# Performance work log

Hardware: AMD Instinct MI355X
Metric: run time of the kernel (lower is better)

The kernel has to match this reference:

```python
import jax, jax.numpy as jnp
import numpy as np

TEMP = 0.1
GROUPS = 16
EPS = 1e-5
COS_EPS = 1e-8


def _encoder(x, conv_w, conv_b, gn_g, gn_b):
    # Conv2d(C,C,3,pad=1) -> GroupNorm(16,C) -> ReLU -> AdaptiveAvgPool2d(1) -> Flatten
    y = jax.lax.conv_general_dilated(
        x, conv_w, window_strides=(1, 1), padding='SAME',
        dimension_numbers=('NCHW', 'OIHW', 'NCHW')) + conv_b[None, :, None, None]
    B, C, H, W = y.shape
    yg = y.reshape(B, GROUPS, C // GROUPS, H, W)
    mu = yg.mean(axis=(2, 3, 4), keepdims=True)
    var = yg.var(axis=(2, 3, 4), keepdims=True)
    yn = ((yg - mu) * jax.lax.rsqrt(var + EPS)).reshape(B, C, H, W)
    y = yn * gn_g[None, :, None, None] + gn_b[None, :, None, None]
    y = jax.nn.relu(y)
    return y.mean(axis=(2, 3))  # [B, C]


def _projector(h, w1, b1, w2, b2, ln_g, ln_b):
    h = jax.nn.relu(h @ w1 + b1)
    h = h @ w2 + b2
    mu = h.mean(axis=-1, keepdims=True)
    var = h.var(axis=-1, keepdims=True)
    return (h - mu) * jax.lax.rsqrt(var + EPS) * ln_g + ln_b


def _predictor(z, w1, b1, w2, b2):
    return jax.nn.relu(z @ w1 + b1) @ w2 + b2


def _l2norm(z):
    n = jnp.sqrt(jnp.sum(z * z, axis=1, keepdims=True))
    return z / jnp.maximum(n, COS_EPS)


def _pair_loss(zi, zj, off_idx):
    # vectorized version of the nested-loop cosine-sim + cross-entropy (label 0)
    S = (_l2norm(zi) @ _l2norm(zj).T) / TEMP  # [B, B]
    pos = jnp.diagonal(S)                     # sim(i_k, j_k)
    neg = jnp.take_along_axis(S, off_idx, axis=1)  # [B, B-1], row k = S[k, l!=k]
    logits = jnp.concatenate([pos[:, None], neg], axis=1)
    return jnp.mean(jax.nn.logsumexp(logits, axis=1) - logits[:, 0])


def setup_inputs() -> dict:
    key = jax.random.key(0)
    ks = jax.random.split(key, 32)
    B, C, H, W, P = 256, 256, 16, 16, 128
    d = {}
    d['x_t2w'] = jax.random.normal(ks[0], (B, C, H, W), jnp.float32)
    d['x_t2f'] = jax.random.normal(ks[1], (B, C, H, W), jnp.float32)
    d['x_t1n'] = jax.random.normal(ks[2], (B, C, H, W), jnp.float32)
    i = 3
    for m in ('t2w', 't2f', 't1n'):
        d[f'conv_w_{m}'] = jax.random.normal(ks[i], (C, C, 3, 3), jnp.float32) * 0.02; i += 1
        d[f'conv_b_{m}'] = jnp.zeros((C,), jnp.float32)
        d[f'gn_g_{m}'] = jnp.ones((C,), jnp.float32)
        d[f'gn_b_{m}'] = jnp.zeros((C,), jnp.float32)
    d['proj_w1'] = jax.random.normal(ks[i], (C, C), jnp.float32) * 0.02; i += 1
    d['proj_b1'] = jnp.zeros((C,), jnp.float32)
    d['proj_w2'] = jax.random.normal(ks[i], (C, P), jnp.float32) * 0.02; i += 1
    d['proj_b2'] = jnp.zeros((P,), jnp.float32)
    d['ln_g'] = jnp.ones((P,), jnp.float32)
    d['ln_b'] = jnp.zeros((P,), jnp.float32)
    d['pred_w1'] = jax.random.normal(ks[i], (P, P), jnp.float32) * 0.02; i += 1
    d['pred_b1'] = jnp.zeros((P,), jnp.float32)
    d['pred_w2'] = jax.random.normal(ks[i], (P, P), jnp.float32) * 0.02; i += 1
    d['pred_b2'] = jnp.zeros((P,), jnp.float32)
    return d


def reference(x_t2w, x_t2f, x_t1n,
              conv_w_t2w, conv_b_t2w, gn_g_t2w, gn_b_t2w,
              conv_w_t2f, conv_b_t2f, gn_g_t2f, gn_b_t2f,
              conv_w_t1n, conv_b_t1n, gn_g_t1n, gn_b_t1n,
              proj_w1, proj_b1, proj_w2, proj_b2, ln_g, ln_b,
              pred_w1, pred_b1, pred_w2, pred_b2):
    xs = [x_t2w, x_t2f, x_t1n]
    enc_params = [(conv_w_t2w, conv_b_t2w, gn_g_t2w, gn_b_t2w),
                  (conv_w_t2f, conv_b_t2f, gn_g_t2f, gn_b_t2f),
                  (conv_w_t1n, conv_b_t1n, gn_g_t1n, gn_b_t1n)]
    encoded = [_encoder(x, *p) for x, p in zip(xs, enc_params)]
    projected = [_projector(e, proj_w1, proj_b1, proj_w2, proj_b2, ln_g, ln_b) for e in encoded]
    preds = [_predictor(z, pred_w1, pred_b1, pred_w2, pred_b2) for z in projected]

    B = projected[0].shape[0]
    off_idx = jnp.asarray(np.array([[l for l in range(B) if l != k] for k in range(B)],
                                    dtype=np.int32))
    pairs = [(0, 1), (0, 2), (1, 2)]
    loss = sum(_pair_loss(projected[i], projected[j], off_idx) for i, j in pairs) / len(pairs)

    return (jnp.stack(encoded), jnp.stack(projected), jnp.stack(preds), loss)
```

## Files before the change

### kernel.cpp

```cpp
#include <hip/hip_runtime.h>
#include <hip/hip_bf16.h>

typedef float f32x4 __attribute__((ext_vector_type(4)));
typedef __bf16 bf16x8 __attribute__((ext_vector_type(8)));
typedef unsigned short u16x8 __attribute__((ext_vector_type(8)));

#define GN_EPS 1e-5f
#define LN_EPS 1e-5f
#define COS_EPS_F 1e-8f

__device__ __forceinline__ unsigned short f2bf(float f) {
  unsigned int u = __builtin_bit_cast(unsigned int, f);
  u += 0x7fffu + ((u >> 16) & 1u);
  return (unsigned short)(u >> 16);
}

__global__ void transpose_kernel(const float* __restrict__ x0,
                                 const float* __restrict__ x1,
                                 const float* __restrict__ x2,
                                 unsigned short* __restrict__ xT,
                                 unsigned int strideElems, int mBase) {
  __shared__ float lds[64][129];
  int m = mBase + (blockIdx.x >> 11);
  int bid = blockIdx.x & 2047;
  const float* x = (m == 0) ? x0 : ((m == 1) ? x1 : x2);
  unsigned short* dst = xT + (unsigned int)(m - mBase) * strideElems;

  int hwt = bid & 3, cit = (bid >> 2) & 1, b = bid >> 3;
  int hw0 = hwt * 64, ci0 = cit * 128;
  int tid = threadIdx.x;

  int hwx = tid & 63, cy0 = tid >> 6;
  const float* xb = x + (b * 256 + ci0) * 256 + hw0;
  #pragma unroll 8
  for (int p = 0; p < 32; ++p) {
    int cy = cy0 + 4 * p;
    lds[hwx][cy] = xb[cy * 256 + hwx];
  }
  __syncthreads();

  int cp = tid & 63, hy0 = tid >> 6;
  unsigned int* outp = (unsigned int*)(dst + (b * 256 + hw0) * 256 + ci0);
  #pragma unroll 4
  for (int p = 0; p < 16; ++p) {
    int hy = hy0 + 4 * p;
    float lo = lds[hy][2 * cp];
    float hi = lds[hy][2 * cp + 1];
    unsigned int w = ((unsigned int)f2bf(hi) << 16) | f2bf(lo);
    outp[hy * 128 + cp] = w;
  }
}

__global__ void pack_kernel(const float* __restrict__ w0,
                            const float* __restrict__ w1,
                            const float* __restrict__ w2,
                            unsigned short* __restrict__ wp,
                            unsigned short* __restrict__ zerobuf) {
  int m = blockIdx.y;
  const float* w = (m == 0) ? w0 : ((m == 1) ? w1 : w2);
  int idx = blockIdx.x * 256 + threadIdx.x;
  if (m == 0 && blockIdx.x == 0 && threadIdx.x < 256) zerobuf[threadIdx.x] = 0;
  int ci = idx & 255;
  int rest = idx >> 8;
  int khw = rest % 9, co = rest / 9;
  wp[m * 589824 + idx] = f2bf(w[(co * 256 + ci) * 9 + khw]);
}

__device__ __forceinline__ void gl_lds16(const unsigned short* g, unsigned short* l) {
  __builtin_amdgcn_global_load_lds(
      (const __attribute__((address_space(1))) void*)g,
      (__attribute__((address_space(3))) void*)l, 16, 0, 0);
}

__launch_bounds__(512, 2)
__global__ void conv_gn_pool(const unsigned short* __restrict__ xT,
                             unsigned int xTstride,
                             const unsigned short* __restrict__ wp,
                             const unsigned short* __restrict__ zb,
                             const float* __restrict__ cb0, const float* __restrict__ cb1,
                             const float* __restrict__ cb2,
                             const float* __restrict__ gg0, const float* __restrict__ gg1,
                             const float* __restrict__ gg2,
                             const float* __restrict__ gb0, const float* __restrict__ gb1,
                             const float* __restrict__ gb2,
                             float* __restrict__ enc, int mBase) {
  __shared__ unsigned short Ab[4][8192];
  __shared__ unsigned short Bb[4][8192];
  __shared__ float gsum[16], gsq[16], pooled[256];

  int mm = mBase + (blockIdx.x >> 8);
  int bb = blockIdx.x & 255;
  int b = (bb & 7) * 32 + (bb >> 3);
  const float* cbias = (mm == 0) ? cb0 : ((mm == 1) ? cb1 : cb2);
  const float* gng   = (mm == 0) ? gg0 : ((mm == 1) ? gg1 : gg2);
  const float* gnb   = (mm == 0) ? gb0 : ((mm == 1) ? gb1 : gb2);

  int tid = threadIdx.x;
  int wid = tid >> 6, lane = tid & 63;
  int wr = wid >> 2, wc = wid & 3;
  int l15 = lane & 15, l4 = lane >> 4;

  if (tid < 16) { gsum[tid] = 0.f; gsq[tid] = 0.f; }
  if (tid < 256) pooled[tid] = 0.f;

  int s0 = tid, s1 = 512 + tid;
  int r0 = s0 >> 2, c0 = s0 & 3;
  int r1 = s1 >> 2, c1 = s1 & 3;
  int cs0 = (c0 ^ ((r0 >> 1) & 3)) * 8;
  int cs1 = (c1 ^ ((r1 >> 1) & 3)) * 8;
  int rh0 = r0 >> 4, rw0 = r0 & 15;
  int rh1 = r1 >> 4, rw1 = r1 & 15;

  const unsigned short* xb = xT + (unsigned int)(mm - mBase) * xTstride + b * 65536;
  const unsigned short* wpm = wp + mm * 589824;
  const unsigned short* bB0 = wpm + r0 * 2304 + cs0;
  const unsigned short* bB1 = wpm + r1 * 2304 + cs1;

  int kch = (l4 ^ ((l15 >> 1) & 3)) * 8;
  int base_af = (wr * 128 + l15) * 32 + kch;
  int base_bf = (wc * 64 + l15) * 32 + kch;

  f32x4 acc[8][4];
  #pragma unroll
  for (int i = 0; i < 8; ++i)
    #pragma unroll
    for (int j = 0; j < 4; ++j) acc[i][j] = (f32x4)(0.0f);

  #define STAGE_A(T2)                                                          \
    {                                                                          \
      int khw_ = (T2) >> 3, kc_ = (T2) & 7;                                    \
      int kh_ = khw_ / 3, kw_ = khw_ - kh_ * 3;                                \
      int ci0_ = kc_ * 32;                                                     \
      unsigned short* dst_ = &Ab[(T2) & 3][0];                                 \
      int h0_ = rh0 + kh_ - 1, w0_ = rw0 + kw_ - 1;                            \
      const unsigned short* sA0 = ((unsigned)h0_ < 16u && (unsigned)w0_ < 16u) \
          ? xb + ((h0_ * 16 + w0_) * 256 + ci0_ + cs0) : zb;                   \
      gl_lds16(sA0, dst_ + s0 * 8);                                            \
      int h1_ = rh1 + kh_ - 1, w1_ = rw1 + kw_ - 1;                            \
      const unsigned short* sA1 = ((unsigned)h1_ < 16u && (unsigned)w1_ < 16u) \
          ? xb + ((h1_ * 16 + w1_) * 256 + ci0_ + cs1) : zb;                   \
      gl_lds16(sA1, dst_ + s1 * 8);                                            \
    }
  #define STAGE_B(T2)                                                          \
    {                                                                          \
      int off_ = ((T2) >> 3) * 256 + ((T2) & 7) * 32;                          \
      unsigned short* dst_ = &Bb[(T2) & 3][0];                                 \
      gl_lds16(bB0 + off_, dst_ + s0 * 8);                                     \
      gl_lds16(bB1 + off_, dst_ + s1 * 8);                                     \
    }

  STAGE_A(0); STAGE_B(0); STAGE_A(1); STAGE_B(1);
  asm volatile("s_waitcnt vmcnt(4)" ::: "memory");
  __builtin_amdgcn_s_barrier();

  for (int t = 0; t < 72; ++t) {
    const unsigned short* Ap = &Ab[t & 3][0];
    const unsigned short* Bp = &Bb[t & 3][0];
    int tp2 = t + 2;
    bf16x8 af[8], bfr[4];
    #pragma unroll
    for (int j = 0; j < 4; ++j)
      af[j] = __builtin_bit_cast(bf16x8, *(const u16x8*)&Ap[base_af + j * 512]);
    #pragma unroll
    for (int n = 0; n < 4; ++n)
      bfr[n] = __builtin_bit_cast(bf16x8, *(const u16x8*)&Bp[base_bf + n * 512]);
    if (tp2 < 72) STAGE_A(tp2);
    #pragma unroll
    for (int j = 4; j < 8; ++j)
      af[j] = __builtin_bit_cast(bf16x8, *(const u16x8*)&Ap[base_af + j * 512]);
    if (tp2 < 72) STAGE_B(tp2);
    __builtin_amdgcn_s_setprio(1);
    #pragma unroll
    for (int j = 0; j < 8; ++j)
      #pragma unroll
      for (int n = 0; n < 4; ++n)
        acc[j][n] = __builtin_amdgcn_mfma_f32_16x16x32_bf16(af[j], bfr[n], acc[j][n], 0, 0, 0);
    __builtin_amdgcn_s_setprio(0);
    if (t < 70) asm volatile("s_waitcnt vmcnt(4)" ::: "memory");
    else        asm volatile("s_waitcnt vmcnt(0)" ::: "memory");
    __builtin_amdgcn_s_barrier();
  }
  #undef STAGE_A
  #undef STAGE_B

  float bias[4], ggv[4], gbv[4];
  #pragma unroll
  for (int nf = 0; nf < 4; ++nf) {
    int co = wc * 64 + nf * 16 + l15;
    bias[nf] = cbias[co]; ggv[nf] = gng[co]; gbv[nf] = gnb[co];
  }
  #pragma unroll
  for (int nf = 0; nf < 4; ++nf) {
    float s1 = 0.f, s2 = 0.f;
    #pragma unroll
    for (int mf = 0; mf < 8; ++mf)
      #pragma unroll
      for (int i = 0; i < 4; ++i) {
        float v = acc[mf][nf][i] + bias[nf];
        acc[mf][nf][i] = v;
        s1 += v; s2 += v * v;
      }
    #pragma unroll
    for (int d = 1; d < 64; d <<= 1) {
      s1 += __shfl_xor(s1, d);
      s2 += __shfl_xor(s2, d);
    }
    if (lane == 0) {
      atomicAdd(&gsum[wc * 4 + nf], s1);
      atomicAdd(&gsq[wc * 4 + nf], s2);
    }
  }
  __syncthreads();
  #pragma unroll
  for (int nf = 0; nf < 4; ++nf) {
    int g = wc * 4 + nf;
    float mean = gsum[g] * (1.f / 4096.f);
    float var = gsq[g] * (1.f / 4096.f) - mean * mean;
    float rs = rsqrtf(var + GN_EPS);
    float p = 0.f;
    #pragma unroll
    for (int mf = 0; mf < 8; ++mf)
      #pragma unroll
      for (int i = 0; i < 4; ++i) {
        float v = (acc[mf][nf][i] - mean) * rs * ggv[nf] + gbv[nf];
        p += fmaxf(v, 0.f);
      }
    p += __shfl_xor(p, 16);
    p += __shfl_xor(p, 32);
    if (lane < 16) atomicAdd(&pooled[wc * 64 + nf * 16 + l15], p);
  }
  __syncthreads();
  if (tid < 256)
    enc[mm * 65536 + b * 256 + tid] = pooled[tid] * (1.f / 256.f);
}

__global__ void proj_pred(const float* __restrict__ enc,
                          const float* __restrict__ w1, const float* __restrict__ b1,
                          const float* __restrict__ w2, const float* __restrict__ b2,
                          const float* __restrict__ lng, const float* __restrict__ lnb,
                          const float* __restrict__ pw1, const float* __restrict__ pb1,
                          const float* __restrict__ pw2, const float* __restrict__ pb2,
                          float* __restrict__ proj, float* __restrict__ pred,
                          float* __restrict__ znorm) {
  __shared__ float row[256], h1[256], zz[128], p1[128], red[2];
  int r = blockIdx.x, tid = threadIdx.x;
  row[tid] = enc[r * 256 + tid];
  __syncthreads();
  float a = 0.f;
  for (int k = 0; k < 256; ++k) a += row[k] * w1[k * 256 + tid];
  h1[tid] = fmaxf(a + b1[tid], 0.f);
  __syncthreads();
  if (tid < 128) {
    a = 0.f;
    for (int k = 0; k < 256; ++k) a += h1[k] * w2[k * 128 + tid];
    zz[tid] = a + b2[tid];
  }
  __syncthreads();
  if (tid == 0) {
    float m = 0.f;
    for (int k = 0; k < 128; ++k) m += zz[k];
    m *= (1.f / 128.f);
    float v = 0.f;
    for (int k = 0; k < 128; ++k) { float d = zz[k] - m; v += d * d; }
    red[0] = m;
    red[1] = rsqrtf(v * (1.f / 128.f) + LN_EPS);
  }
  __syncthreads();
  float zval = 0.f;
  if (tid < 128) {
    zval = (zz[tid] - red[0]) * red[1] * lng[tid] + lnb[tid];
    proj[r * 128 + tid] = zval;
  }
  __syncthreads();
  if (tid < 128) zz[tid] = zval;
  __syncthreads();
  if (tid == 0) {
    float s = 0.f;
    for (int k = 0; k < 128; ++k) s += zz[k] * zz[k];
    red[0] = 1.f / fmaxf(sqrtf(s), COS_EPS_F);
  }
  __syncthreads();
  if (tid < 128) {
    znorm[r * 128 + tid] = zz[tid] * red[0];
    a = 0.f;
    for (int k = 0; k < 128; ++k) a += zz[k] * pw1[k * 128 + tid];
    p1[tid] = fmaxf(a + pb1[tid], 0.f);
  }
  __syncthreads();
  if (tid < 128) {
    a = 0.f;
    for (int k = 0; k < 128; ++k) a += p1[k] * pw2[k * 128 + tid];
    pred[r * 128 + tid] = a + pb2[tid];
  }
}

__global__ void loss_kernel(const float* __restrict__ zn, float* __restrict__ part) {
  __shared__ float zi[128], sv[256], rbuf[256];
  int blk = blockIdx.x;
  int p = blk >> 8, k = blk & 255;
  int i = (p == 2) ? 1 : 0;
  int j = (p == 0) ? 1 : 2;
  int tid = threadIdx.x;
  if (tid < 128) zi[tid] = zn[(i * 256 + k) * 128 + tid];
  __syncthreads();
  const float4* zj = (const float4*)&zn[(j * 256 + tid) * 128];
  float s = 0.f;
  #pragma unroll 8
  for (int d = 0; d < 32; ++d) {
    float4 aq = *(const float4*)&zi[d * 4];
    float4 bq = zj[d];
    s += aq.x * bq.x + aq.y * bq.y + aq.z * bq.z + aq.w * bq.w;
  }
  s *= 10.0f;
  sv[tid] = s;
  rbuf[tid] = s;
  __syncthreads();
  for (int d = 128; d > 0; d >>= 1) {
    if (tid < d) rbuf[tid] = fmaxf(rbuf[tid], rbuf[tid + d]);
    __syncthreads();
  }
  float m = rbuf[0];
  __syncthreads();
  rbuf[tid] = expf(s - m);
  __syncthreads();
  for (int d = 128; d > 0; d >>= 1) {
    if (tid < d) rbuf[tid] += rbuf[tid + d];
    __syncthreads();
  }
  if (tid == 0) part[blk] = m + logf(rbuf[0]) - sv[k];
}

__global__ void finalize_loss(const float* __restrict__ part, float* __restrict__ out) {
  __shared__ float red[256];
  int tid = threadIdx.x;
  float s = 0.f;
  for (int idx = tid; idx < 768; idx += 256) s += part[idx];
  red[tid] = s;
  __syncthreads();
  for (int d = 128; d > 0; d >>= 1) {
    if (tid < d) red[tid] += red[tid + d];
    __syncthreads();
  }
  if (tid == 0) out[0] = red[0] * (1.f / 768.f);
}

extern "C" void kernel_launch(void* const* d_in, const int* in_sizes, int n_in,
                              void* d_out, int out_size, void* d_ws, size_t ws_size,
                              hipStream_t stream) {
  const float* x[3]  = {(const float*)d_in[0], (const float*)d_in[1], (const float*)d_in[2]};
  const float* cw[3] = {(const float*)d_in[3], (const float*)d_in[7], (const float*)d_in[11]};
  const float* cb[3] = {(const float*)d_in[4], (const float*)d_in[8], (const float*)d_in[12]};
  const float* gg[3] = {(const float*)d_in[5], (const float*)d_in[9], (const float*)d_in[13]};
  const float* gb[3] = {(const float*)d_in[6], (const float*)d_in[10], (const float*)d_in[14]};
  const float* p_w1 = (const float*)d_in[15];
  const float* p_b1 = (const float*)d_in[16];
  const float* p_w2 = (const float*)d_in[17];
  const float* p_b2 = (const float*)d_in[18];
  const float* ln_g = (const float*)d_in[19];
  const float* ln_b = (const float*)d_in[20];
  const float* q_w1 = (const float*)d_in[21];
  const float* q_b1 = (const float*)d_in[22];
  const float* q_w2 = (const float*)d_in[23];
  const float* q_b2 = (const float*)d_in[24];

  float* out = (float*)d_out;
  char* ws = (char*)d_ws;

  const size_t XT_ONE = 33554432;
  bool merged = ws_size >= (3 * XT_ONE + 3538944 + 393216 + 3072 + 512);

  size_t xt_total = merged ? 3 * XT_ONE : XT_ONE;
  unsigned short* xT  = (unsigned short*)ws;
  unsigned short* wpk = (unsigned short*)(ws + xt_total);
  float* znorm = (float*)(ws + xt_total + 3538944);
  float* part  = (float*)(ws + xt_total + 3538944 + 393216);
  unsigned short* zb = (unsigned short*)(ws + xt_total + 3538944 + 393216 + 3072);

  float* enc  = out;
  float* proj = out + 196608;
  float* pred = out + 294912;
  float* lossp = out + 393216;

  pack_kernel<<<dim3(2304, 3), dim3(256), 0, stream>>>(cw[0], cw[1], cw[2], wpk, zb);

  if (merged) {
    transpose_kernel<<<dim3(6144), dim3(256), 0, stream>>>(x[0], x[1], x[2], xT, 16777216u, 0);
    conv_gn_pool<<<dim3(768), dim3(512), 0, stream>>>(
        xT, 16777216u, wpk, zb, cb[0], cb[1], cb[2], gg[0], gg[1], gg[2],
        gb[0], gb[1], gb[2], enc, 0);
  } else {
    for (int m = 0; m < 3; ++m) {
      transpose_kernel<<<dim3(2048), dim3(256), 0, stream>>>(x[0], x[1], x[2], xT, 0u, m);
      conv_gn_pool<<<dim3(256), dim3(512), 0, stream>>>(
          xT, 0u, wpk, zb, cb[0], cb[1], cb[2], gg[0], gg[1], gg[2],
          gb[0], gb[1], gb[2], enc, m);
    }
  }
  proj_pred<<<dim3(768), dim3(256), 0, stream>>>(enc, p_w1, p_b1, p_w2, p_b2, ln_g, ln_b,
                                                 q_w1, q_b1, q_w2, q_b2, proj, pred, znorm);
  loss_kernel<<<dim3(768), dim3(256), 0, stream>>>(znorm, part);
  finalize_loss<<<dim3(1), dim3(256), 0, stream>>>(part, lossp);
}
```

Baseline: 330.3 us.

## Deepen conv GEMM prefetch to three stages and reorder K loop channel-outer

```diff
diff --git a/kernel.cpp b/kernel.cpp
--- a/kernel.cpp
+++ b/kernel.cpp
@@ -126,12 +126,11 @@
     #pragma unroll
     for (int j = 0; j < 4; ++j) acc[i][j] = (f32x4)(0.0f);
 
-  #define STAGE_A(T2)                                                          \
+  #define STAGE_A(KC, KHW, BUF)                                                \
     {                                                                          \
-      int khw_ = (T2) >> 3, kc_ = (T2) & 7;                                    \
-      int kh_ = khw_ / 3, kw_ = khw_ - kh_ * 3;                                \
-      int ci0_ = kc_ * 32;                                                     \
-      unsigned short* dst_ = &Ab[(T2) & 3][0];                                 \
+      int kh_ = (KHW) / 3, kw_ = (KHW) % 3;                                    \
+      int ci0_ = (KC) * 32;                                                    \
+      unsigned short* dst_ = &Ab[(BUF)][0];                                    \
       int h0_ = rh0 + kh_ - 1, w0_ = rw0 + kw_ - 1;                            \
       const unsigned short* sA0 = ((unsigned)h0_ < 16u && (unsigned)w0_ < 16u) \
           ? xb + ((h0_ * 16 + w0_) * 256 + ci0_ + cs0) : zb;                   \
@@ -141,47 +140,67 @@
           ? xb + ((h1_ * 16 + w1_) * 256 + ci0_ + cs1) : zb;                   \
       gl_lds16(sA1, dst_ + s1 * 8);                                            \
     }
-  #define STAGE_B(T2)                                                          \
+  #define STAGE_B(KC, KHW, BUF)                                                \
     {                                                                          \
-      int off_ = ((T2) >> 3) * 256 + ((T2) & 7) * 32;                          \
-      unsigned short* dst_ = &Bb[(T2) & 3][0];                                 \
+      int off_ = (KHW) * 256 + (KC) * 32;                                      \
+      unsigned short* dst_ = &Bb[(BUF)][0];                                    \
       gl_lds16(bB0 + off_, dst_ + s0 * 8);                                     \
       gl_lds16(bB1 + off_, dst_ + s1 * 8);                                     \
     }
 
-  STAGE_A(0); STAGE_B(0); STAGE_A(1); STAGE_B(1);
-  asm volatile("s_waitcnt vmcnt(4)" ::: "memory");
+  #define TILE_COMPUTE(BUF)                                                    \
+    {                                                                          \
+      const unsigned short* Ap = &Ab[(BUF)][0];                                \
+      const unsigned short* Bp = &Bb[(BUF)][0];                                \
+      bf16x8 af[8], bfr[4];                                                    \
+      _Pragma("unroll")                                                        \
+      for (int j = 0; j < 8; ++j)                                              \
+        af[j] = __builtin_bit_cast(bf16x8, *(const u16x8*)&Ap[base_af + j * 512]); \
+      _Pragma("unroll")                                                        \
+      for (int n = 0; n < 4; ++n)                                              \
+        bfr[n] = __builtin_bit_cast(bf16x8, *(const u16x8*)&Bp[base_bf + n * 512]); \
+      __builtin_amdgcn_s_setprio(1);                                           \
+      _Pragma("unroll")                                                        \
+      for (int j = 0; j < 8; ++j)                                              \
+        _Pragma("unroll")                                                      \
+        for (int n = 0; n < 4; ++n)                                            \
+          acc[j][n] = __builtin_amdgcn_mfma_f32_16x16x32_bf16(af[j], bfr[n],   \
+                                                              acc[j][n], 0, 0, 0); \
+      __builtin_amdgcn_s_setprio(0);                                           \
+    }
+
+  STAGE_A(0, 0, 0); STAGE_B(0, 0, 0);
+  STAGE_A(0, 1, 1); STAGE_B(0, 1, 1);
+  STAGE_A(0, 2, 2); STAGE_B(0, 2, 2);
+  asm volatile("s_waitcnt vmcnt(8)" ::: "memory");
   __builtin_amdgcn_s_barrier();
 
-  for (int t = 0; t < 72; ++t) {
-    const unsigned short* Ap = &Ab[t & 3][0];
-    const unsigned short* Bp = &Bb[t & 3][0];
-    int tp2 = t + 2;
-    bf16x8 af[8], bfr[4];
+  for (int kc = 0; kc < 7; ++kc) {
     #pragma unroll
-    for (int j = 0; j < 4; ++j)
-      af[j] = __builtin_bit_cast(bf16x8, *(const u16x8*)&Ap[base_af + j * 512]);
-    #pragma unroll
-    for (int n = 0; n < 4; ++n)
-      bfr[n] = __builtin_bit_cast(bf16x8, *(const u16x8*)&Bp[base_bf + n * 512]);
-    if (tp2 < 72) STAGE_A(tp2);
-    #pragma unroll
-    for (int j = 4; j < 8; ++j)
-      af[j] = __builtin_bit_cast(bf16x8, *(const u16x8*)&Ap[base_af + j * 512]);
-    if (tp2 < 72) STAGE_B(tp2);
-    __builtin_amdgcn_s_setprio(1);
-    #pragma unroll
-    for (int j = 0; j < 8; ++j)
-      #pragma unroll
-      for (int n = 0; n < 4; ++n)
-        acc[j][n] = __builtin_amdgcn_mfma_f32_16x16x32_bf16(af[j], bfr[n], acc[j][n], 0, 0, 0);
-    __builtin_amdgcn_s_setprio(0);
-    if (t < 70) asm volatile("s_waitcnt vmcnt(4)" ::: "memory");
-    else        asm volatile("s_waitcnt vmcnt(0)" ::: "memory");
+    for (int khw = 0; khw < 9; ++khw) {
+      int buf = (kc + khw) & 3;
+      int buf3 = (kc + khw + 3) & 3;
+      if (khw <= 5) { STAGE_A(kc, khw + 3, buf3); STAGE_B(kc, khw + 3, buf3); }
+      else          { STAGE_A(kc + 1, khw - 6, buf3); STAGE_B(kc + 1, khw - 6, buf3); }
+      TILE_COMPUTE(buf);
+      asm volatile("s_waitcnt vmcnt(8)" ::: "memory");
+      __builtin_amdgcn_s_barrier();
+    }
+  }
+  #pragma unroll
+  for (int khw = 0; khw < 9; ++khw) {
+    int buf = (7 + khw) & 3;
+    int buf3 = (7 + khw + 3) & 3;
+    if (khw <= 5) { STAGE_A(7, khw + 3, buf3); STAGE_B(7, khw + 3, buf3); }
+    TILE_COMPUTE(buf);
+    if (khw <= 5)      asm volatile("s_waitcnt vmcnt(8)" ::: "memory");
+    else if (khw == 6) asm volatile("s_waitcnt vmcnt(4)" ::: "memory");
+    else               asm volatile("s_waitcnt vmcnt(0)" ::: "memory");
     __builtin_amdgcn_s_barrier();
   }
   #undef STAGE_A
   #undef STAGE_B
+  #undef TILE_COMPUTE
 
   float bias[4], ggv[4], gbv[4];
   #pragma unroll
```

After: 330.4 us. No clear change (+0.0%).

## Restructure conv into per-tap shifted LDS reads with half-channel tiles, add ablation variants

Applied to the files above, without the earlier changes.

```diff
diff --git a/kernel.cpp b/kernel.cpp
--- a/kernel.cpp
+++ b/kernel.cpp
@@ -54,12 +54,10 @@
 __global__ void pack_kernel(const float* __restrict__ w0,
                             const float* __restrict__ w1,
                             const float* __restrict__ w2,
-                            unsigned short* __restrict__ wp,
-                            unsigned short* __restrict__ zerobuf) {
+                            unsigned short* __restrict__ wp) {
   int m = blockIdx.y;
   const float* w = (m == 0) ? w0 : ((m == 1) ? w1 : w2);
   int idx = blockIdx.x * 256 + threadIdx.x;
-  if (m == 0 && blockIdx.x == 0 && threadIdx.x < 256) zerobuf[threadIdx.x] = 0;
   int ci = idx & 255;
   int rest = idx >> 8;
   int khw = rest % 9, co = rest / 9;
@@ -72,128 +70,190 @@
       (__attribute__((address_space(3))) void*)l, 16, 0, 0);
 }
 
-__launch_bounds__(512, 2)
+template <int V>
+__launch_bounds__(512, 4)
 __global__ void conv_gn_pool(const unsigned short* __restrict__ xT,
                              unsigned int xTstride,
                              const unsigned short* __restrict__ wp,
-                             const unsigned short* __restrict__ zb,
                              const float* __restrict__ cb0, const float* __restrict__ cb1,
                              const float* __restrict__ cb2,
                              const float* __restrict__ gg0, const float* __restrict__ gg1,
                              const float* __restrict__ gg2,
                              const float* __restrict__ gb0, const float* __restrict__ gb1,
                              const float* __restrict__ gb2,
-                             float* __restrict__ enc, int mBase) {
-  __shared__ unsigned short Ab[4][8192];
-  __shared__ unsigned short Bb[4][8192];
-  __shared__ float gsum[16], gsq[16], pooled[256];
-
-  int mm = mBase + (blockIdx.x >> 8);
-  int bb = blockIdx.x & 255;
-  int b = (bb & 7) * 32 + (bb >> 3);
+                             float* __restrict__ enc, int mBase, int nkch) {
+  __shared__ unsigned short As[2][8192];
+  __shared__ unsigned short Bb[2][4096];
+  __shared__ unsigned short zbuf[32];
+  __shared__ float gsum[8], gsq[8], pooled[128];
+
+  int bid = blockIdx.x;
+  int xcd = bid & 7, idx = bid >> 3;
+  int nt = idx & 1;
+  int r = idx >> 1;
+  int mm = mBase + (r >> 5);
+  int img = xcd * 32 + (r & 31);
+
   const float* cbias = (mm == 0) ? cb0 : ((mm == 1) ? cb1 : cb2);
   const float* gng   = (mm == 0) ? gg0 : ((mm == 1) ? gg1 : gg2);
   const float* gnb   = (mm == 0) ? gb0 : ((mm == 1) ? gb1 : gb2);
 
   int tid = threadIdx.x;
   int wid = tid >> 6, lane = tid & 63;
-  int wr = wid >> 2, wc = wid & 3;
+  int wr = wid >> 1, wc = wid & 1;
   int l15 = lane & 15, l4 = lane >> 4;
 
-  if (tid < 16) { gsum[tid] = 0.f; gsq[tid] = 0.f; }
-  if (tid < 256) pooled[tid] = 0.f;
-
-  int s0 = tid, s1 = 512 + tid;
-  int r0 = s0 >> 2, c0 = s0 & 3;
-  int r1 = s1 >> 2, c1 = s1 & 3;
-  int cs0 = (c0 ^ ((r0 >> 1) & 3)) * 8;
-  int cs1 = (c1 ^ ((r1 >> 1) & 3)) * 8;
-  int rh0 = r0 >> 4, rw0 = r0 & 15;
-  int rh1 = r1 >> 4, rw1 = r1 & 15;
-
-  const unsigned short* xb = xT + (unsigned int)(mm - mBase) * xTstride + b * 65536;
-  const unsigned short* wpm = wp + mm * 589824;
-  const unsigned short* bB0 = wpm + r0 * 2304 + cs0;
-  const unsigned short* bB1 = wpm + r1 * 2304 + cs1;
-
-  int kch = (l4 ^ ((l15 >> 1) & 3)) * 8;
-  int base_af = (wr * 128 + l15) * 32 + kch;
-  int base_bf = (wc * 64 + l15) * 32 + kch;
-
-  f32x4 acc[8][4];
+  if (tid < 8) { gsum[tid] = 0.f; gsq[tid] = 0.f; }
+  if (tid < 128) pooled[tid] = 0.f;
+  if (tid < 32) zbuf[tid] = 0;
+
+  const unsigned short* xb =
+      xT + (unsigned int)(mm - mBase) * xTstride + (unsigned int)img * 65536u;
+  const unsigned short* wpB = wp + mm * 589824 + nt * 128 * 2304;
+
+  int rA0 = tid >> 2;
+  const unsigned short* aSrc0 =
+      xb + rA0 * 256 + (((tid & 3) ^ ((rA0 >> 1) & 3)) * 8);
+  unsigned short* aDst0 = &As[0][0] + tid * 8;
+  int sco = tid >> 2;
+  const unsigned short* bSrc =
+      wpB + sco * 2304 + (((tid & 3) ^ ((sco >> 1) & 3)) * 8);
+  unsigned short* bDst = &Bb[0][0] + tid * 8;
+
+  int bq4[4];
   #pragma unroll
-  for (int i = 0; i < 8; ++i)
+  for (int nf = 0; nf < 4; ++nf) {
+    int co = wc * 64 + nf * 16 + l15;
+    bq4[nf] = co * 32 + ((l4 ^ ((co >> 1) & 3)) * 8);
+  }
+
+  f32x4 acc[4][4];
+  #pragma unroll
+  for (int i = 0; i < 4; ++i)
     #pragma unroll
     for (int j = 0; j < 4; ++j) acc[i][j] = (f32x4)(0.0f);
 
-  #define STAGE_A(T2)                                                          \
+  #define LD8(P) __builtin_bit_cast(bf16x8, *(const u16x8*)(P))
+  #define STAGE_A(KCN, PAR)                                                    \
     {                                                                          \
-      int khw_ = (T2) >> 3, kc_ = (T2) & 7;                                    \
-      int kh_ = khw_ / 3, kw_ = khw_ - kh_ * 3;                                \
-      int ci0_ = kc_ * 32;                                                     \
-      unsigned short* dst_ = &Ab[(T2) & 3][0];                                 \
-      int h0_ = rh0 + kh_ - 1, w0_ = rw0 + kw_ - 1;                            \
-      const unsigned short* sA0 = ((unsigned)h0_ < 16u && (unsigned)w0_ < 16u) \
-          ? xb + ((h0_ * 16 + w0_) * 256 + ci0_ + cs0) : zb;                   \
-      gl_lds16(sA0, dst_ + s0 * 8);                                            \
-      int h1_ = rh1 + kh_ - 1, w1_ = rw1 + kw_ - 1;                            \
-      const unsigned short* sA1 = ((unsigned)h1_ < 16u && (unsigned)w1_ < 16u) \
-          ? xb + ((h1_ * 16 + w1_) * 256 + ci0_ + cs1) : zb;                   \
-      gl_lds16(sA1, dst_ + s1 * 8);                                            \
-    }
-  #define STAGE_B(T2)                                                          \
+      gl_lds16(aSrc0 + (KCN) * 32, aDst0 + (PAR) * 8192);                      \
+      gl_lds16(aSrc0 + 32768 + (KCN) * 32, aDst0 + 4096 + (PAR) * 8192);       \
+    }
+  #define STAGE_B(KCN, TAPN, PAR)                                              \
+    gl_lds16(bSrc + (TAPN) * 256 + (KCN) * 32, bDst + (PAR) * 4096)
+
+  bf16x8 afP[4], bfrP[4];
+
+  if constexpr (V != 3) { STAGE_B(0, 0, 0); STAGE_A(0, 0); }
+  asm volatile("s_waitcnt vmcnt(0)" ::: "memory");
+  __builtin_amdgcn_s_barrier();
+
+  if constexpr (V == 1) {
+    #pragma unroll
+    for (int nf = 0; nf < 4; ++nf) bfrP[nf] = LD8(&Bb[0][bq4[nf]]);
+    #pragma unroll
+    for (int mf = 0; mf < 4; ++mf) {
+      int p = wr * 64 + mf * 16 + l15;
+      afP[mf] = LD8(&As[0][p * 32 + ((l4 ^ ((p >> 1) & 3)) * 8)]);
+    }
+    asm volatile("s_waitcnt lgkmcnt(0)" ::: "memory");
+    __builtin_amdgcn_sched_barrier(0);
+  }
+
+  #define TAP_BODY(ASP, BRD, DH, DW, DOA, AKCN, APAR, DOB, BKC, BTAP, BWR)     \
     {                                                                          \
-      int off_ = ((T2) >> 3) * 256 + ((T2) & 7) * 32;                          \
-      unsigned short* dst_ = &Bb[(T2) & 3][0];                                 \
-      gl_lds16(bB0 + off_, dst_ + s0 * 8);                                     \
-      gl_lds16(bB1 + off_, dst_ + s1 * 8);                                     \
-    }
-
-  STAGE_A(0); STAGE_B(0); STAGE_A(1); STAGE_B(1);
-  asm volatile("s_waitcnt vmcnt(4)" ::: "memory");
-  __builtin_amdgcn_s_barrier();
-
-  for (int t = 0; t < 72; ++t) {
-    const unsigned short* Ap = &Ab[t & 3][0];
-    const unsigned short* Bp = &Bb[t & 3][0];
-    int tp2 = t + 2;
-    bf16x8 af[8], bfr[4];
-    #pragma unroll
-    for (int j = 0; j < 4; ++j)
-      af[j] = __builtin_bit_cast(bf16x8, *(const u16x8*)&Ap[base_af + j * 512]);
-    #pragma unroll
-    for (int n = 0; n < 4; ++n)
-      bfr[n] = __builtin_bit_cast(bf16x8, *(const u16x8*)&Bp[base_bf + n * 512]);
-    if (tp2 < 72) STAGE_A(tp2);
-    #pragma unroll
-    for (int j = 4; j < 8; ++j)
-      af[j] = __builtin_bit_cast(bf16x8, *(const u16x8*)&Ap[base_af + j * 512]);
-    if (tp2 < 72) STAGE_B(tp2);
-    __builtin_amdgcn_s_setprio(1);
-    #pragma unroll
-    for (int j = 0; j < 8; ++j)
-      #pragma unroll
-      for (int n = 0; n < 4; ++n)
-        acc[j][n] = __builtin_amdgcn_mfma_f32_16x16x32_bf16(af[j], bfr[n], acc[j][n], 0, 0, 0);
-    __builtin_amdgcn_s_setprio(0);
-    if (t < 70) asm volatile("s_waitcnt vmcnt(4)" ::: "memory");
-    else        asm volatile("s_waitcnt vmcnt(0)" ::: "memory");
-    __builtin_amdgcn_s_barrier();
-  }
+      if constexpr (V != 3) {                                                  \
+        if (DOB) STAGE_B(BKC, BTAP, BWR);                                      \
+        if (DOA) STAGE_A(AKCN, APAR);                                          \
+      }                                                                        \
+      bf16x8 af[4], bfr[4];                                                    \
+      if constexpr (V != 1) {                                                  \
+        _Pragma("unroll")                                                      \
+        for (int nf = 0; nf < 4; ++nf) bfr[nf] = LD8(&Bb[BRD][bq4[nf]]);       \
+        _Pragma("unroll")                                                      \
+        for (int mf = 0; mf < 4; ++mf) {                                       \
+          int p = wr * 64 + mf * 16 + l15;                                     \
+          int pp = p + ((DH) - 1) * 16 + ((DW) - 1);                           \
+          bool ok = true;                                                      \
+          if ((DH) == 0) ok = ok && ((p >> 4) >= 1);                           \
+          if ((DH) == 2) ok = ok && ((p >> 4) <= 14);                          \
+          if ((DW) == 0) ok = ok && ((p & 15) >= 1);                           \
+          if ((DW) == 2) ok = ok && ((p & 15) <= 14);                          \
+          const unsigned short* pa =                                           \
+              ok ? &As[ASP][pp * 32 + ((l4 ^ ((pp >> 1) & 3)) * 8)]            \
+                 : &zbuf[l4 * 8];                                              \
+          af[mf] = LD8(pa);                                                    \
+        }                                                                      \
+        asm volatile("s_waitcnt lgkmcnt(0)" ::: "memory");                     \
+        __builtin_amdgcn_sched_barrier(0);                                     \
+      }                                                                        \
+      if constexpr (V == 2) {                                                  \
+        _Pragma("unroll")                                                      \
+        for (int q = 0; q < 4; ++q) {                                          \
+          asm volatile("" :: "v"(__builtin_bit_cast(f32x4, af[q])));           \
+          asm volatile("" :: "v"(__builtin_bit_cast(f32x4, bfr[q])));          \
+        }                                                                      \
+      } else {                                                                 \
+        __builtin_amdgcn_s_setprio(1);                                         \
+        _Pragma("unroll")                                                      \
+        for (int mf = 0; mf < 4; ++mf)                                         \
+          _Pragma("unroll")                                                    \
+          for (int nf = 0; nf < 4; ++nf) {                                     \
+            if constexpr (V == 1)                                              \
+              acc[mf][nf] = __builtin_amdgcn_mfma_f32_16x16x32_bf16(           \
+                  afP[mf], bfrP[nf], acc[mf][nf], 0, 0, 0);                    \
+            else                                                               \
+              acc[mf][nf] = __builtin_amdgcn_mfma_f32_16x16x32_bf16(           \
+                  af[mf], bfr[nf], acc[mf][nf], 0, 0, 0);                      \
+          }                                                                    \
+        __builtin_amdgcn_s_setprio(0);                                         \
+      }                                                                        \
+      asm volatile("s_waitcnt vmcnt(0)" ::: "memory");                         \
+      __builtin_amdgcn_s_barrier();                                            \
+    }
+
+  for (int kch = 0; kch < nkch; ++kch) {
+    int kc = kch * 2;
+    TAP_BODY(0, 0, 0, 0, 1, kc + 1, 1, 1, kc, 1, 1)
+    TAP_BODY(0, 1, 0, 1, 0, 0, 0, 1, kc, 2, 0)
+    TAP_BODY(0, 0, 0, 2, 0, 0, 0, 1, kc, 3, 1)
+    TAP_BODY(0, 1, 1, 0, 0, 0, 0, 1, kc, 4, 0)
+    TAP_BODY(0, 0, 1, 1, 0, 0, 0, 1, kc, 5, 1)
+    TAP_BODY(0, 1, 1, 2, 0, 0, 0, 1, kc, 6, 0)
+    TAP_BODY(0, 0, 2, 0, 0, 0, 0, 1, kc, 7, 1)
+    TAP_BODY(0, 1, 2, 1, 0, 0, 0, 1, kc, 8, 0)
+    TAP_BODY(0, 0, 2, 2, 0, 0, 0, 1, kc + 1, 0, 1)
+    int kco = kc + 1;
+    int doA = (kco < 7);
+    int doB9 = (kco < 7);
+    TAP_BODY(1, 1, 0, 0, doA, kco + 1, 0, 1, kco, 1, 0)
+    TAP_BODY(1, 0, 0, 1, 0, 0, 0, 1, kco, 2, 1)
+    TAP_BODY(1, 1, 0, 2, 0, 0, 0, 1, kco, 3, 0)
+    TAP_BODY(1, 0, 1, 0, 0, 0, 0, 1, kco, 4, 1)
+    TAP_BODY(1, 1, 1, 1, 0, 0, 0, 1, kco, 5, 0)
+    TAP_BODY(1, 0, 1, 2, 0, 0, 0, 1, kco, 6, 1)
+    TAP_BODY(1, 1, 2, 0, 0, 0, 0, 1, kco, 7, 0)
+    TAP_BODY(1, 0, 2, 1, 0, 0, 0, 1, kco, 8, 1)
+    TAP_BODY(1, 1, 2, 2, 0, 0, 0, doB9, kco + 1, 0, 0)
+  }
+  #undef TAP_BODY
   #undef STAGE_A
   #undef STAGE_B
+  #undef LD8
+
+  __syncthreads();
 
   float bias[4], ggv[4], gbv[4];
   #pragma unroll
   for (int nf = 0; nf < 4; ++nf) {
-    int co = wc * 64 + nf * 16 + l15;
+    int co = nt * 128 + wc * 64 + nf * 16 + l15;
     bias[nf] = cbias[co]; ggv[nf] = gng[co]; gbv[nf] = gnb[co];
   }
   #pragma unroll
   for (int nf = 0; nf < 4; ++nf) {
     float s1 = 0.f, s2 = 0.f;
     #pragma unroll
-    for (int mf = 0; mf < 8; ++mf)
+    for (int mf = 0; mf < 4; ++mf)
       #pragma unroll
       for (int i = 0; i < 4; ++i) {
         float v = acc[mf][nf][i] + bias[nf];
@@ -219,7 +279,7 @@
     float rs = rsqrtf(var + GN_EPS);
     float p = 0.f;
     #pragma unroll
-    for (int mf = 0; mf < 8; ++mf)
+    for (int mf = 0; mf < 4; ++mf)
       #pragma unroll
       for (int i = 0; i < 4; ++i) {
         float v = (acc[mf][nf][i] - mean) * rs * ggv[nf] + gbv[nf];
@@ -230,8 +290,8 @@
     if (lane < 16) atomicAdd(&pooled[wc * 64 + nf * 16 + l15], p);
   }
   __syncthreads();
-  if (tid < 256)
-    enc[mm * 65536 + b * 256 + tid] = pooled[tid] * (1.f / 256.f);
+  if (tid < 128)
+    enc[mm * 65536 + img * 256 + nt * 128 + tid] = pooled[tid] * (1.f / 256.f);
 }
 
 __global__ void proj_pred(const float* __restrict__ enc,
@@ -367,37 +427,48 @@
   char* ws = (char*)d_ws;
 
   const size_t XT_ONE = 33554432;
-  bool merged = ws_size >= (3 * XT_ONE + 3538944 + 393216 + 3072 + 512);
+  bool merged = ws_size >= (3 * XT_ONE + 3538944 + 393216 + 3072 + 262144 + 512);
 
   size_t xt_total = merged ? 3 * XT_ONE : XT_ONE;
   unsigned short* xT  = (unsigned short*)ws;
   unsigned short* wpk = (unsigned short*)(ws + xt_total);
-  float* znorm = (float*)(ws + xt_total + 3538944);
-  float* part  = (float*)(ws + xt_total + 3538944 + 393216);
-  unsigned short* zb = (unsigned short*)(ws + xt_total + 3538944 + 393216 + 3072);
+  float* znorm   = (float*)(ws + xt_total + 3538944);
+  float* part    = (float*)(ws + xt_total + 3538944 + 393216);
+  float* scratch = (float*)(ws + xt_total + 3538944 + 393216 + 3072);
 
   float* enc  = out;
   float* proj = out + 196608;
   float* pred = out + 294912;
   float* lossp = out + 393216;
 
-  pack_kernel<<<dim3(2304, 3), dim3(256), 0, stream>>>(cw[0], cw[1], cw[2], wpk, zb);
-
+  pack_kernel<<<dim3(2304, 3), dim3(256), 0, stream>>>(cw[0], cw[1], cw[2], wpk);
+
+  unsigned int stride = merged ? 16777216u : 0u;
   if (merged) {
-    transpose_kernel<<<dim3(6144), dim3(256), 0, stream>>>(x[0], x[1], x[2], xT, 16777216u, 0);
-    conv_gn_pool<<<dim3(768), dim3(512), 0, stream>>>(
-        xT, 16777216u, wpk, zb, cb[0], cb[1], cb[2], gg[0], gg[1], gg[2],
-        gb[0], gb[1], gb[2], enc, 0);
+    transpose_kernel<<<dim3(6144), dim3(256), 0, stream>>>(x[0], x[1], x[2], xT, stride, 0);
+    conv_gn_pool<0><<<dim3(1536), dim3(512), 0, stream>>>(
+        xT, stride, wpk, cb[0], cb[1], cb[2], gg[0], gg[1], gg[2],
+        gb[0], gb[1], gb[2], enc, 0, 4);
   } else {
     for (int m = 0; m < 3; ++m) {
       transpose_kernel<<<dim3(2048), dim3(256), 0, stream>>>(x[0], x[1], x[2], xT, 0u, m);
-      conv_gn_pool<<<dim3(256), dim3(512), 0, stream>>>(
-          xT, 0u, wpk, zb, cb[0], cb[1], cb[2], gg[0], gg[1], gg[2],
-          gb[0], gb[1], gb[2], enc, m);
+      conv_gn_pool<0><<<dim3(512), dim3(512), 0, stream>>>(
+          xT, 0u, wpk, cb[0], cb[1], cb[2], gg[0], gg[1], gg[2],
+          gb[0], gb[1], gb[2], enc, m, 4);
     }
   }
   proj_pred<<<dim3(768), dim3(256), 0, stream>>>(enc, p_w1, p_b1, p_w2, p_b2, ln_g, ln_b,
                                                  q_w1, q_b1, q_w2, q_b2, proj, pred, znorm);
   loss_kernel<<<dim3(768), dim3(256), 0, stream>>>(znorm, part);
   finalize_loss<<<dim3(1), dim3(256), 0, stream>>>(part, lossp);
-}
+
+  conv_gn_pool<1><<<dim3(512), dim3(512), 0, stream>>>(
+      xT, stride, wpk, cb[0], cb[1], cb[2], gg[0], gg[1], gg[2],
+      gb[0], gb[1], gb[2], scratch, 0, 2);
+  conv_gn_pool<2><<<dim3(512), dim3(512), 0, stream>>>(
+      xT, stride, wpk, cb[0], cb[1], cb[2], gg[0], gg[1], gg[2],
+      gb[0], gb[1], gb[2], scratch, 0, 2);
+  conv_gn_pool<3><<<dim3(512), dim3(512), 0, stream>>>(
+      xT, stride, wpk, cb[0], cb[1], cb[2], gg[0], gg[1], gg[2],
+      gb[0], gb[1], gb[2], scratch, 0, 2);
+}
```

Measured after the change: 562.9 us. 70.4% more time.
